# Kernel optimization log

Measured on AMD Instinct MI355X. Metric: run time of the kernel, lower is better.

Reference implementation:

```python
import jax, jax.numpy as jnp
import numpy as np


def setup_inputs() -> dict:
    key = jax.random.key(0)
    k1, k2, k3 = jax.random.split(key, 3)
    B, C, H, W = 64, 512, 28, 28
    K = 32
    std = 1.0 / (K * C) ** 0.5
    x = jax.random.normal(k1, (B, C, H, W), dtype=jnp.float32)
    codewords = jax.random.uniform(k2, (K, C), dtype=jnp.float32, minval=-std, maxval=std)
    scale = jax.random.uniform(k3, (K,), dtype=jnp.float32, minval=-1.0, maxval=0.0)
    return {"x": x, "codewords": codewords, "scale": scale}


def reference(x, codewords, scale):
    # x: (B, C, H, W) -> descriptors (B, N, C)
    B, C, H, W = x.shape
    K = codewords.shape[0]
    xd = x.reshape(B, C, H * W).transpose(0, 2, 1)  # (B, N, C)

    # scaled L2: scale_k * ||x_n - c_k||^2, expanded without (B,N,K,C) intermediate
    x_sq = jnp.sum(xd * xd, axis=-1, keepdims=True)            # (B, N, 1)
    c_sq = jnp.sum(codewords * codewords, axis=-1)             # (K,)
    xc = jnp.einsum("bnc,kc->bnk", xd, codewords)              # (B, N, K)
    dist = scale * (x_sq - 2.0 * xc + c_sq)                    # (B, N, K)

    A = jax.nn.softmax(dist, axis=2)                           # (B, N, K)

    # encoded_k = sum_n A[b,n,k] * (x[b,n] - c[k])
    wx = jnp.einsum("bnk,bnc->bkc", A, xd)                     # (B, K, C)
    wsum = jnp.sum(A, axis=1)                                  # (B, K)
    encoded = wx - wsum[:, :, None] * codewords[None, :, :]    # (B, K, C)
    return encoded
```

## Files before the change

kernel.cpp:

```cpp
#include <hip/hip_runtime.h>

#define BB 64
#define CC 512
#define NPIX 784
#define KK 32
#define NSA 13
#define AS 800
#define CW_S 520
#define NSTEP 24

typedef __attribute__((ext_vector_type(8))) short short8;
typedef __attribute__((ext_vector_type(4))) float floatx4;
typedef __attribute__((ext_vector_type(4))) unsigned short ushort4v;

#define WSUM_OFF (BB * KK * AS)

__device__ __forceinline__ unsigned short f2bf(float f) {
    union { float f; unsigned u; } v; v.f = f;
    return (unsigned short)((v.u + 0x7FFFu + ((v.u >> 16) & 1u)) >> 16);
}
__device__ __forceinline__ float bf2f(unsigned short h) {
    union { unsigned u; float f; } v; v.u = ((unsigned)h) << 16; return v.f;
}
__device__ __forceinline__ short8 pack8(const float4& a, const float4& b) {
    short8 r;
    r[0] = (short)f2bf(a.x); r[1] = (short)f2bf(a.y);
    r[2] = (short)f2bf(a.z); r[3] = (short)f2bf(a.w);
    r[4] = (short)f2bf(b.x); r[5] = (short)f2bf(b.y);
    r[6] = (short)f2bf(b.z); r[7] = (short)f2bf(b.w);
    return r;
}

__global__ __launch_bounds__(256, 4) void kA(const float* __restrict__ x,
                                             const float* __restrict__ cw,
                                             const float* __restrict__ scale,
                                             unsigned short* __restrict__ Ag)
{
    __shared__ __align__(16) unsigned short cs[KK * CW_S];
    __shared__ float csq_p[8][KK];
    __shared__ float csq_l[KK];
    __shared__ float wredA[4][KK];

    const int t    = threadIdx.x;
    const int lane = t & 63, w = t >> 6;
    const int col  = lane & 15, quad = lane >> 4;
    const int split = blockIdx.x, b = blockIdx.y;
    const int p0    = (split < 12) ? split * 64 : 720;

    if (split == 0 && t < 64) {
        const short8 z = {0, 0, 0, 0, 0, 0, 0, 0};
        const int k = t >> 1, off = (t & 1) * 8;
        *(short8*)&Ag[(size_t)b * KK * AS + (size_t)k * AS + NPIX + off] = z;
    }

#pragma unroll 4
    for (int j = 0; j < 16; ++j) {
        const int qidx = t + j * 256;
        const int row = qidx >> 7, qc = qidx & 127;
        const float4 v = *(const float4*)&cw[row * CC + qc * 4];
        ushort4v p; p.x = f2bf(v.x); p.y = f2bf(v.y); p.z = f2bf(v.z); p.w = f2bf(v.w);
        *(ushort4v*)&cs[row * CW_S + qc * 4] = p;
    }
    __syncthreads();
    {
        const int k = t & 31, part = t >> 5;
        float s = 0.f;
        for (int i = 0; i < 64; ++i) {
            const float v = bf2f(cs[k * CW_S + part * 64 + i]);
            s += v * v;
        }
        csq_p[part][k] = s;
    }
    __syncthreads();
    if (t < KK) {
        float s = 0.f;
#pragma unroll
        for (int p = 0; p < 8; ++p) s += csq_p[p][t];
        csq_l[t] = s;
    }
    __syncthreads();

    const float s0 = scale[col], s1 = scale[col + 16];
    const float q0 = csq_l[col], q1 = csq_l[col + 16];

    const int px = p0 + w * 16 + col;
    const float* xb = x + (size_t)b * CC * NPIX + px;

    floatx4 acc0 = {0.f, 0.f, 0.f, 0.f};
    floatx4 acc1 = {0.f, 0.f, 0.f, 0.f};
    float xsqp = 0.f;
    float va[8], vb[8];

#pragma unroll
    for (int j = 0; j < 8; ++j) va[j] = xb[(size_t)(quad * 8 + j) * NPIX];

#pragma unroll
    for (int kc = 0; kc < 16; kc += 2) {
        {
            const int cb = (kc + 1) * 32 + quad * 8;
#pragma unroll
            for (int j = 0; j < 8; ++j) vb[j] = xb[(size_t)(cb + j) * NPIX];
        }
        {
#pragma unroll
            for (int j = 0; j < 8; ++j) xsqp += va[j] * va[j];
            short8 a;
#pragma unroll
            for (int j = 0; j < 8; ++j) a[j] = (short)f2bf(va[j]);
            const int cb0 = kc * 32 + quad * 8;
            const short8 b0 = *(const short8*)&cs[col * CW_S + cb0];
            const short8 b1 = *(const short8*)&cs[(col + 16) * CW_S + cb0];
            acc0 = __builtin_amdgcn_mfma_f32_16x16x32_bf16(a, b0, acc0, 0, 0, 0);
            acc1 = __builtin_amdgcn_mfma_f32_16x16x32_bf16(a, b1, acc1, 0, 0, 0);
        }
        if (kc + 2 < 16) {
            const int cb = (kc + 2) * 32 + quad * 8;
#pragma unroll
            for (int j = 0; j < 8; ++j) va[j] = xb[(size_t)(cb + j) * NPIX];
        }
        {
#pragma unroll
            for (int j = 0; j < 8; ++j) xsqp += vb[j] * vb[j];
            short8 a;
#pragma unroll
            for (int j = 0; j < 8; ++j) a[j] = (short)f2bf(vb[j]);
            const int cb1 = (kc + 1) * 32 + quad * 8;
            const short8 b0 = *(const short8*)&cs[col * CW_S + cb1];
            const short8 b1 = *(const short8*)&cs[(col + 16) * CW_S + cb1];
            acc0 = __builtin_amdgcn_mfma_f32_16x16x32_bf16(a, b0, acc0, 0, 0, 0);
            acc1 = __builtin_amdgcn_mfma_f32_16x16x32_bf16(a, b1, acc1, 0, 0, 0);
        }
    }

    xsqp += __shfl_xor(xsqp, 16);
    xsqp += __shfl_xor(xsqp, 32);

    unsigned short* Ab = Ag + (size_t)b * KK * AS + p0 + w * 16;
    float ts0 = 0.f, ts1 = 0.f;
#pragma unroll
    for (int r = 0; r < 4; ++r) {
        const float xq = __shfl(xsqp, quad * 4 + r);
        const float d0 = s0 * (xq + q0 - 2.f * acc0[r]);
        const float d1 = s1 * (xq + q1 - 2.f * acc1[r]);
        float mx = fmaxf(d0, d1);
        mx = fmaxf(mx, __shfl_xor(mx, 1));
        mx = fmaxf(mx, __shfl_xor(mx, 2));
        mx = fmaxf(mx, __shfl_xor(mx, 4));
        mx = fmaxf(mx, __shfl_xor(mx, 8));
        const float e0 = __expf(d0 - mx), e1 = __expf(d1 - mx);
        float sm = e0 + e1;
        sm += __shfl_xor(sm, 1);
        sm += __shfl_xor(sm, 2);
        sm += __shfl_xor(sm, 4);
        sm += __shfl_xor(sm, 8);
        const float inv = 1.f / sm;
        const float a0 = e0 * inv, a1 = e1 * inv;
        Ab[col * AS + quad * 4 + r]        = f2bf(a0);
        Ab[(col + 16) * AS + quad * 4 + r] = f2bf(a1);
        ts0 += a0; ts1 += a1;
    }

    ts0 += __shfl_xor(ts0, 16); ts0 += __shfl_xor(ts0, 32);
    ts1 += __shfl_xor(ts1, 16); ts1 += __shfl_xor(ts1, 32);
    if (quad == 0) { wredA[w][col] = ts0; wredA[w][col + 16] = ts1; }
    __syncthreads();
    if (t < KK) {
        float s;
        if (split < 12) s = wredA[0][t] + wredA[1][t] + wredA[2][t] + wredA[3][t];
        else            s = wredA[3][t];
        float* wsf = (float*)(Ag + WSUM_OFF);
        wsf[(size_t)(split * BB + b) * KK + t] = s;
    }
}

__global__ __launch_bounds__(256) void kB(const float* __restrict__ x,
                                          const float* __restrict__ cw,
                                          const unsigned short* __restrict__ Ag,
                                          float* __restrict__ out)
{
    __shared__ float wsum_l[KK];

    const int t    = threadIdx.x;
    const int lane = t & 63, w = t >> 6;
    const int col  = lane & 15, quad = lane >> 4;
    const int cch  = blockIdx.x, b = blockIdx.y;

    const unsigned short* Ab = Ag + (size_t)b * KK * AS;

    if (t < KK) {
        const float* wsf = (const float*)(Ag + WSUM_OFF);
        float s = 0.f;
#pragma unroll
        for (int sp = 0; sp < NSA; ++sp) s += wsf[(size_t)(sp * BB + b) * KK + t];
        wsum_l[t] = s;
    }

    const int c = cch * 64 + w * 16 + col;
    const float* xp = x + ((size_t)b * CC + c) * NPIX;
    const unsigned short* a0p = Ab + (size_t)col * AS;
    const unsigned short* a1p = Ab + (size_t)(col + 16) * AS;
    const int qo = quad * 8;

    floatx4 acc0 = {0.f, 0.f, 0.f, 0.f};
    floatx4 acc1 = {0.f, 0.f, 0.f, 0.f};
#pragma unroll 6
    for (int s = 0; s < NSTEP; ++s) {
        const int off = s * 32 + qo;
        const short8 av0 = *(const short8*)&a0p[off];
        const short8 av1 = *(const short8*)&a1p[off];
        const float4 xv0 = *(const float4*)&xp[off];
        const float4 xv1 = *(const float4*)&xp[off + 4];
        const short8 bv = pack8(xv0, xv1);
        acc0 = __builtin_amdgcn_mfma_f32_16x16x32_bf16(av0, bv, acc0, 0, 0, 0);
        acc1 = __builtin_amdgcn_mfma_f32_16x16x32_bf16(av1, bv, acc1, 0, 0, 0);
    }
    {
        const int off = NSTEP * 32 + qo;
        const short8 av0 = *(const short8*)&a0p[off];
        const short8 av1 = *(const short8*)&a1p[off];
        float4 xv0 = make_float4(0.f, 0.f, 0.f, 0.f);
        float4 xv1 = make_float4(0.f, 0.f, 0.f, 0.f);
        if (quad < 2) {
            xv0 = *(const float4*)&xp[off];
            xv1 = *(const float4*)&xp[off + 4];
        }
        const short8 bv = pack8(xv0, xv1);
        acc0 = __builtin_amdgcn_mfma_f32_16x16x32_bf16(av0, bv, acc0, 0, 0, 0);
        acc1 = __builtin_amdgcn_mfma_f32_16x16x32_bf16(av1, bv, acc1, 0, 0, 0);
    }

    __syncthreads();

    float* ob = out + (size_t)b * KK * CC + c;
    const float* cp = cw + c;
#pragma unroll
    for (int r = 0; r < 4; ++r) {
        const int k0 = quad * 4 + r;
        ob[(size_t)k0 * CC]        = acc0[r] - wsum_l[k0]      * cp[(size_t)k0 * CC];
        ob[(size_t)(k0 + 16) * CC] = acc1[r] - wsum_l[k0 + 16] * cp[(size_t)(k0 + 16) * CC];
    }
}

extern "C" void kernel_launch(void* const* d_in, const int* in_sizes, int n_in,
                              void* d_out, int out_size, void* d_ws, size_t ws_size,
                              hipStream_t stream) {
    const float* x     = (const float*)d_in[0];
    const float* cw    = (const float*)d_in[1];
    const float* scale = (const float*)d_in[2];
    float* out = (float*)d_out;
    unsigned short* Ag = (unsigned short*)d_ws;

    kA<<<dim3(NSA, BB), dim3(256), 0, stream>>>(x, cw, scale, Ag);
    kB<<<dim3(8, BB), dim3(256), 0, stream>>>(x, cw, Ag, out);
}
```

Baseline: 182.8 us.

## Stage x tiles through double-buffered LDS and read codewords directly from global

The distance kernel now loads x with coalesced float4 reads into a double-buffered, padded LDS tile. Each wave reads its MFMA A-operands from that tile, and the next 64-channel chunk is prefetched into registers while the current one is used. The shared-memory bf16 copy of the codewords is dropped. Codeword fragments are now read from global memory (expected to hit cache) and converted to bf16 at every step, and the codeword norms are computed from fp32 values. This aims to replace the strided per-pixel global loads of x with wide coalesced transfers. The cost is one barrier per chunk and repeated codeword conversion work.

Result: slower. 193.9 us (+6.1%).

```diff
diff --git a/kernel.cpp b/kernel.cpp
--- a/kernel.cpp
+++ b/kernel.cpp
@@ -6,21 +6,18 @@
 #define KK 32
 #define NSA 13
 #define AS 800
-#define CW_S 520
 #define NSTEP 24
+#define RS 66
+#define XT_BUF (64*RS)
 
 typedef __attribute__((ext_vector_type(8))) short short8;
 typedef __attribute__((ext_vector_type(4))) float floatx4;
-typedef __attribute__((ext_vector_type(4))) unsigned short ushort4v;
 
 #define WSUM_OFF (BB * KK * AS)
 
 __device__ __forceinline__ unsigned short f2bf(float f) {
     union { float f; unsigned u; } v; v.f = f;
     return (unsigned short)((v.u + 0x7FFFu + ((v.u >> 16) & 1u)) >> 16);
-}
-__device__ __forceinline__ float bf2f(unsigned short h) {
-    union { unsigned u; float f; } v; v.u = ((unsigned)h) << 16; return v.f;
 }
 __device__ __forceinline__ short8 pack8(const float4& a, const float4& b) {
     short8 r;
@@ -36,7 +33,7 @@
                                              const float* __restrict__ scale,
                                              unsigned short* __restrict__ Ag)
 {
-    __shared__ __align__(16) unsigned short cs[KK * CW_S];
+    __shared__ __align__(16) float xt[2 * XT_BUF];
     __shared__ float csq_p[8][KK];
     __shared__ float csq_l[KK];
     __shared__ float wredA[4][KK];
@@ -53,21 +50,25 @@
         *(short8*)&Ag[(size_t)b * KK * AS + (size_t)k * AS + NPIX + off] = z;
     }
 
-#pragma unroll 4
-    for (int j = 0; j < 16; ++j) {
-        const int qidx = t + j * 256;
-        const int row = qidx >> 7, qc = qidx & 127;
-        const float4 v = *(const float4*)&cw[row * CC + qc * 4];
-        ushort4v p; p.x = f2bf(v.x); p.y = f2bf(v.y); p.z = f2bf(v.z); p.w = f2bf(v.w);
-        *(ushort4v*)&cs[row * CW_S + qc * 4] = p;
-    }
-    __syncthreads();
+    const float* xb = x + (size_t)b * CC * NPIX + p0;
+    const int r0 = t >> 4, p4 = t & 15;
+
+#pragma unroll
+    for (int j = 0; j < 4; ++j) {
+        const int row = r0 + j * 16;
+        const float4 v = *(const float4*)&xb[(size_t)row * NPIX + p4 * 4];
+        float* d = &xt[row * RS + p4 * 4];
+        *(float2*)&d[0] = make_float2(v.x, v.y);
+        *(float2*)&d[2] = make_float2(v.z, v.w);
+    }
     {
         const int k = t & 31, part = t >> 5;
+        const float* cp = cw + k * CC + part * 64;
         float s = 0.f;
-        for (int i = 0; i < 64; ++i) {
-            const float v = bf2f(cs[k * CW_S + part * 64 + i]);
-            s += v * v;
+#pragma unroll
+        for (int i = 0; i < 16; ++i) {
+            const float4 v = *(const float4*)&cp[i * 4];
+            s += v.x * v.x + v.y * v.y + v.z * v.z + v.w * v.w;
         }
         csq_p[part][k] = s;
     }
@@ -78,62 +79,57 @@
         for (int p = 0; p < 8; ++p) s += csq_p[p][t];
         csq_l[t] = s;
     }
-    __syncthreads();
-
-    const float s0 = scale[col], s1 = scale[col + 16];
-    const float q0 = csq_l[col], q1 = csq_l[col + 16];
-
-    const int px = p0 + w * 16 + col;
-    const float* xb = x + (size_t)b * CC * NPIX + px;
 
     floatx4 acc0 = {0.f, 0.f, 0.f, 0.f};
     floatx4 acc1 = {0.f, 0.f, 0.f, 0.f};
     float xsqp = 0.f;
-    float va[8], vb[8];
-
-#pragma unroll
-    for (int j = 0; j < 8; ++j) va[j] = xb[(size_t)(quad * 8 + j) * NPIX];
-
-#pragma unroll
-    for (int kc = 0; kc < 16; kc += 2) {
-        {
-            const int cb = (kc + 1) * 32 + quad * 8;
-#pragma unroll
-            for (int j = 0; j < 8; ++j) vb[j] = xb[(size_t)(cb + j) * NPIX];
-        }
-        {
-#pragma unroll
-            for (int j = 0; j < 8; ++j) xsqp += va[j] * va[j];
+    const int wcol = w * 16 + col;
+
+#pragma unroll
+    for (int ch = 0; ch < 8; ++ch) {
+        const int cur = ch & 1;
+        float4 pre[4];
+        if (ch < 7) {
+            const float* xs = xb + (size_t)(ch + 1) * 64 * NPIX;
+#pragma unroll
+            for (int j = 0; j < 4; ++j)
+                pre[j] = *(const float4*)&xs[(size_t)(r0 + j * 16) * NPIX + p4 * 4];
+        }
+#pragma unroll
+        for (int kl = 0; kl < 2; ++kl) {
+            const int kcg = ch * 2 + kl;
+            float va[8];
+            const float* src = &xt[cur * XT_BUF + (kl * 32 + quad * 8) * RS + wcol];
+#pragma unroll
+            for (int j = 0; j < 8; ++j) va[j] = src[j * RS];
             short8 a;
 #pragma unroll
-            for (int j = 0; j < 8; ++j) a[j] = (short)f2bf(va[j]);
-            const int cb0 = kc * 32 + quad * 8;
-            const short8 b0 = *(const short8*)&cs[col * CW_S + cb0];
-            const short8 b1 = *(const short8*)&cs[(col + 16) * CW_S + cb0];
+            for (int j = 0; j < 8; ++j) { xsqp += va[j] * va[j]; a[j] = (short)f2bf(va[j]); }
+            const int cb = kcg * 32 + quad * 8;
+            const short8 b0 = pack8(*(const float4*)&cw[col * CC + cb],
+                                    *(const float4*)&cw[col * CC + cb + 4]);
+            const short8 b1 = pack8(*(const float4*)&cw[(col + 16) * CC + cb],
+                                    *(const float4*)&cw[(col + 16) * CC + cb + 4]);
             acc0 = __builtin_amdgcn_mfma_f32_16x16x32_bf16(a, b0, acc0, 0, 0, 0);
             acc1 = __builtin_amdgcn_mfma_f32_16x16x32_bf16(a, b1, acc1, 0, 0, 0);
         }
-        if (kc + 2 < 16) {
-            const int cb = (kc + 2) * 32 + quad * 8;
-#pragma unroll
-            for (int j = 0; j < 8; ++j) va[j] = xb[(size_t)(cb + j) * NPIX];
-        }
-        {
-#pragma unroll
-            for (int j = 0; j < 8; ++j) xsqp += vb[j] * vb[j];
-            short8 a;
-#pragma unroll
-            for (int j = 0; j < 8; ++j) a[j] = (short)f2bf(vb[j]);
-            const int cb1 = (kc + 1) * 32 + quad * 8;
-            const short8 b0 = *(const short8*)&cs[col * CW_S + cb1];
-            const short8 b1 = *(const short8*)&cs[(col + 16) * CW_S + cb1];
-            acc0 = __builtin_amdgcn_mfma_f32_16x16x32_bf16(a, b0, acc0, 0, 0, 0);
-            acc1 = __builtin_amdgcn_mfma_f32_16x16x32_bf16(a, b1, acc1, 0, 0, 0);
+        if (ch < 7) {
+            const int nb = cur ^ 1;
+#pragma unroll
+            for (int j = 0; j < 4; ++j) {
+                float* d = &xt[nb * XT_BUF + (r0 + j * 16) * RS + p4 * 4];
+                *(float2*)&d[0] = make_float2(pre[j].x, pre[j].y);
+                *(float2*)&d[2] = make_float2(pre[j].z, pre[j].w);
+            }
+            __syncthreads();
         }
     }
 
     xsqp += __shfl_xor(xsqp, 16);
     xsqp += __shfl_xor(xsqp, 32);
+
+    const float s0 = scale[col], s1 = scale[col + 16];
+    const float q0 = csq_l[col], q1 = csq_l[col + 16];
 
     unsigned short* Ab = Ag + (size_t)b * KK * AS + p0 + w * 16;
     float ts0 = 0.f, ts1 = 0.f;
```

## Switch kA to 32x32x16 MFMA with 128-pixel blocks

Applied to the files above, without the earlier changes.

Kernel A now uses one 32x32x16 bf16 MFMA per wave covering 32 pixels and all 32 codewords, instead of two 16x16x32 MFMAs over 16 pixels. Each block now covers 128 pixels, so the grid goes from 13 to 7 splits per batch. The last split is overlapped at pixel 656, with three of its waves idle and the overlapping rows left out of the weight-sum count. The aim is fewer, larger MFMAs and fewer blocks, at the cost of 16-lane softmax shuffles across 32 lanes and idle waves in the tail block.

Result: no change. 181.3 us (-0.8%).

```diff
diff --git a/kernel.cpp b/kernel.cpp
--- a/kernel.cpp
+++ b/kernel.cpp
@@ -4,13 +4,14 @@
 #define CC 512
 #define NPIX 784
 #define KK 32
-#define NSA 13
+#define NSA 7
 #define AS 800
 #define CW_S 520
 #define NSTEP 24
 
 typedef __attribute__((ext_vector_type(8))) short short8;
 typedef __attribute__((ext_vector_type(4))) float floatx4;
+typedef __attribute__((ext_vector_type(16))) float floatx16;
 typedef __attribute__((ext_vector_type(4))) unsigned short ushort4v;
 
 #define WSUM_OFF (BB * KK * AS)
@@ -43,9 +44,10 @@
 
     const int t    = threadIdx.x;
     const int lane = t & 63, w = t >> 6;
-    const int col  = lane & 15, quad = lane >> 4;
+    const int pl   = lane & 31, h = lane >> 5;
     const int split = blockIdx.x, b = blockIdx.y;
-    const int p0    = (split < 12) ? split * 64 : 720;
+    const int p0    = (split < 6) ? split * 128 : 656;
+    const bool active = !(split == 6 && w < 3);
 
     if (split == 0 && t < 64) {
         const short8 z = {0, 0, 0, 0, 0, 0, 0, 0};
@@ -80,94 +82,82 @@
     }
     __syncthreads();
 
-    const float s0 = scale[col], s1 = scale[col + 16];
-    const float q0 = csq_l[col], q1 = csq_l[col + 16];
-
-    const int px = p0 + w * 16 + col;
+    const float sk = scale[pl];
+    const float qk = csq_l[pl];
+
+    const int px = p0 + w * 32 + pl;
     const float* xb = x + (size_t)b * CC * NPIX + px;
 
-    floatx4 acc0 = {0.f, 0.f, 0.f, 0.f};
-    floatx4 acc1 = {0.f, 0.f, 0.f, 0.f};
+    floatx16 acc = {0.f,0.f,0.f,0.f,0.f,0.f,0.f,0.f,0.f,0.f,0.f,0.f,0.f,0.f,0.f,0.f};
     float xsqp = 0.f;
-    float va[8], vb[8];
-
-#pragma unroll
-    for (int j = 0; j < 8; ++j) va[j] = xb[(size_t)(quad * 8 + j) * NPIX];
-
-#pragma unroll
-    for (int kc = 0; kc < 16; kc += 2) {
-        {
-            const int cb = (kc + 1) * 32 + quad * 8;
-#pragma unroll
-            for (int j = 0; j < 8; ++j) vb[j] = xb[(size_t)(cb + j) * NPIX];
-        }
-        {
-#pragma unroll
-            for (int j = 0; j < 8; ++j) xsqp += va[j] * va[j];
-            short8 a;
-#pragma unroll
-            for (int j = 0; j < 8; ++j) a[j] = (short)f2bf(va[j]);
-            const int cb0 = kc * 32 + quad * 8;
-            const short8 b0 = *(const short8*)&cs[col * CW_S + cb0];
-            const short8 b1 = *(const short8*)&cs[(col + 16) * CW_S + cb0];
-            acc0 = __builtin_amdgcn_mfma_f32_16x16x32_bf16(a, b0, acc0, 0, 0, 0);
-            acc1 = __builtin_amdgcn_mfma_f32_16x16x32_bf16(a, b1, acc1, 0, 0, 0);
-        }
-        if (kc + 2 < 16) {
-            const int cb = (kc + 2) * 32 + quad * 8;
-#pragma unroll
-            for (int j = 0; j < 8; ++j) va[j] = xb[(size_t)(cb + j) * NPIX];
-        }
-        {
-#pragma unroll
-            for (int j = 0; j < 8; ++j) xsqp += vb[j] * vb[j];
-            short8 a;
-#pragma unroll
-            for (int j = 0; j < 8; ++j) a[j] = (short)f2bf(vb[j]);
-            const int cb1 = (kc + 1) * 32 + quad * 8;
-            const short8 b0 = *(const short8*)&cs[col * CW_S + cb1];
-            const short8 b1 = *(const short8*)&cs[(col + 16) * CW_S + cb1];
-            acc0 = __builtin_amdgcn_mfma_f32_16x16x32_bf16(a, b0, acc0, 0, 0, 0);
-            acc1 = __builtin_amdgcn_mfma_f32_16x16x32_bf16(a, b1, acc1, 0, 0, 0);
-        }
-    }
-
-    xsqp += __shfl_xor(xsqp, 16);
-    xsqp += __shfl_xor(xsqp, 32);
-
-    unsigned short* Ab = Ag + (size_t)b * KK * AS + p0 + w * 16;
-    float ts0 = 0.f, ts1 = 0.f;
-#pragma unroll
-    for (int r = 0; r < 4; ++r) {
-        const float xq = __shfl(xsqp, quad * 4 + r);
-        const float d0 = s0 * (xq + q0 - 2.f * acc0[r]);
-        const float d1 = s1 * (xq + q1 - 2.f * acc1[r]);
-        float mx = fmaxf(d0, d1);
-        mx = fmaxf(mx, __shfl_xor(mx, 1));
-        mx = fmaxf(mx, __shfl_xor(mx, 2));
-        mx = fmaxf(mx, __shfl_xor(mx, 4));
-        mx = fmaxf(mx, __shfl_xor(mx, 8));
-        const float e0 = __expf(d0 - mx), e1 = __expf(d1 - mx);
-        float sm = e0 + e1;
-        sm += __shfl_xor(sm, 1);
-        sm += __shfl_xor(sm, 2);
-        sm += __shfl_xor(sm, 4);
-        sm += __shfl_xor(sm, 8);
-        const float inv = 1.f / sm;
-        const float a0 = e0 * inv, a1 = e1 * inv;
-        Ab[col * AS + quad * 4 + r]        = f2bf(a0);
-        Ab[(col + 16) * AS + quad * 4 + r] = f2bf(a1);
-        ts0 += a0; ts1 += a1;
-    }
-
-    ts0 += __shfl_xor(ts0, 16); ts0 += __shfl_xor(ts0, 32);
-    ts1 += __shfl_xor(ts1, 16); ts1 += __shfl_xor(ts1, 32);
-    if (quad == 0) { wredA[w][col] = ts0; wredA[w][col + 16] = ts1; }
+
+    if (active) {
+        float va[8], vb[8];
+#pragma unroll
+        for (int j = 0; j < 8; ++j) va[j] = xb[(size_t)(h * 8 + j) * NPIX];
+
+#pragma unroll
+        for (int kc = 0; kc < 32; kc += 2) {
+            {
+                const int cb = (kc + 1) * 16 + h * 8;
+#pragma unroll
+                for (int j = 0; j < 8; ++j) vb[j] = xb[(size_t)(cb + j) * NPIX];
+            }
+            {
+                short8 a;
+#pragma unroll
+                for (int j = 0; j < 8; ++j) { xsqp += va[j] * va[j]; a[j] = (short)f2bf(va[j]); }
+                const short8 bf = *(const short8*)&cs[pl * CW_S + kc * 16 + h * 8];
+                acc = __builtin_amdgcn_mfma_f32_32x32x16_bf16(a, bf, acc, 0, 0, 0);
+            }
+            if (kc + 2 < 32) {
+                const int cb = (kc + 2) * 16 + h * 8;
+#pragma unroll
+                for (int j = 0; j < 8; ++j) va[j] = xb[(size_t)(cb + j) * NPIX];
+            }
+            {
+                short8 a;
+#pragma unroll
+                for (int j = 0; j < 8; ++j) { xsqp += vb[j] * vb[j]; a[j] = (short)f2bf(vb[j]); }
+                const short8 bf = *(const short8*)&cs[pl * CW_S + (kc + 1) * 16 + h * 8];
+                acc = __builtin_amdgcn_mfma_f32_32x32x16_bf16(a, bf, acc, 0, 0, 0);
+            }
+        }
+    }
+
+    const float xsqf = xsqp + __shfl_xor(xsqp, 32);
+
+    unsigned short* Ab = Ag + (size_t)b * KK * AS + p0 + w * 32;
+    float ts = 0.f;
+    if (active) {
+#pragma unroll
+        for (int r = 0; r < 16; ++r) {
+            const int pwr = (r & 3) + 8 * (r >> 2) + 4 * h;
+            const float xq = __shfl(xsqf, pwr);
+            const float d = sk * (xq + qk - 2.f * acc[r]);
+            float mx = d;
+            mx = fmaxf(mx, __shfl_xor(mx, 1));
+            mx = fmaxf(mx, __shfl_xor(mx, 2));
+            mx = fmaxf(mx, __shfl_xor(mx, 4));
+            mx = fmaxf(mx, __shfl_xor(mx, 8));
+            mx = fmaxf(mx, __shfl_xor(mx, 16));
+            const float e = __expf(d - mx);
+            float sm = e;
+            sm += __shfl_xor(sm, 1);
+            sm += __shfl_xor(sm, 2);
+            sm += __shfl_xor(sm, 4);
+            sm += __shfl_xor(sm, 8);
+            sm += __shfl_xor(sm, 16);
+            const float av = e * (1.f / sm);
+            Ab[pl * AS + pwr] = f2bf(av);
+            if (split < 6 || r >= 8) ts += av;
+        }
+    }
+    ts += __shfl_xor(ts, 32);
+    if (lane < 32) wredA[w][pl] = active ? ts : 0.f;
     __syncthreads();
     if (t < KK) {
-        float s;
-        if (split < 12) s = wredA[0][t] + wredA[1][t] + wredA[2][t] + wredA[3][t];
-        else            s = wredA[3][t];
+        const float s = wredA[0][t] + wredA[1][t] + wredA[2][t] + wredA[3][t];
         float* wsf = (float*)(Ag + WSUM_OFF);
         wsf[(size_t)(split * BB + b) * KK + t] = s;
     }
```
